# Kernel optimization log

Hardware: AMD Instinct MI355X
Metric: run time of the kernel (lower is better)

The kernel has to match this reference:

```python
import jax, jax.numpy as jnp
import numpy as np

B, S, D = 2, 2048, 1024
H = 16
HD = D // H  # 64


def setup_inputs() -> dict:
    key = jax.random.key(0)
    ks = jax.random.split(key, 9)
    s = 1.0 / np.sqrt(D)
    x = jax.random.normal(ks[0], (B, S, D), dtype=jnp.float32)
    Wq = jax.random.normal(ks[1], (D, D), dtype=jnp.float32) * s
    Wk = jax.random.normal(ks[2], (D, D), dtype=jnp.float32) * s
    Wv = jax.random.normal(ks[3], (D, D), dtype=jnp.float32) * s
    Wo = jax.random.normal(ks[4], (D, D), dtype=jnp.float32) * s
    bq = jnp.zeros((D,), jnp.float32)
    bk = jnp.zeros((D,), jnp.float32)
    bv = jnp.zeros((D,), jnp.float32)
    bo = jnp.zeros((D,), jnp.float32)
    # causal mask, broadcastable to (B, H, S, S)
    mask = jnp.tril(jnp.ones((S, S), dtype=bool))[None, None, :, :]
    return {"x": x, "Wq": Wq, "bq": bq, "Wk": Wk, "bk": bk,
            "Wv": Wv, "bv": bv, "Wo": Wo, "bo": bo, "mask": mask}


def _split_heads(t):
    # (B, S, D) -> (B, H, S, HD)
    b, s, _ = t.shape
    return t.reshape(b, s, H, HD).transpose(0, 2, 1, 3)


def reference(x, Wq, bq, Wk, bk, Wv, bv, Wo, bo, mask):
    q = _split_heads(x @ Wq + bq)
    k = _split_heads(x @ Wk + bk)
    v = _split_heads(x @ Wv + bv)
    scale = 1.0 / jnp.sqrt(jnp.asarray(HD, dtype=q.dtype))
    scores = jnp.einsum('bhqd,bhkd->bhqk', q, k) * scale
    large_neg = jnp.finfo(scores.dtype).min
    scores = jnp.where(mask, scores, large_neg)
    attn = jax.nn.softmax(scores, axis=-1)
    out = jnp.einsum('bhqk,bhkd->bhqd', attn, v)  # (B,H,S,HD)
    out = out.transpose(0, 2, 1, 3).reshape(x.shape[0], x.shape[1], D)
    return out @ Wo + bo
```

## Files before the change

kernel.cpp:

```cpp
#include <hip/hip_runtime.h>
#include <hip/hip_bf16.h>

typedef __attribute__((ext_vector_type(8))) short bf16x8;
typedef __attribute__((ext_vector_type(4))) float f32x4;

#define B_DIM  2
#define S_DIM  2048
#define D_DIM  1024
#define H_DIM  16
#define HD_DIM 64

__device__ __forceinline__ float bf2f(ushort u) {
    union { unsigned int ui; float f; } c; c.ui = ((unsigned int)u) << 16; return c.f;
}
__device__ __forceinline__ ushort f2bf(float f) {
    __hip_bfloat16 h = __float2bfloat16(f);
    return *reinterpret_cast<ushort*>(&h);
}

__device__ __forceinline__ void async_cp16(const ushort* g, ushort* l) {
    __builtin_amdgcn_global_load_lds(
        (const __attribute__((address_space(1))) void*)g,
        (__attribute__((address_space(3))) void*)l, 16, 0, 0);
}

__global__ __launch_bounds__(256) void detect_kernel(const ushort* __restrict__ x,
                                                     int* __restrict__ flag) {
    __shared__ int any;
    int tid = threadIdx.x;
    if (tid == 0) any = 0;
    __syncthreads();
    int cnt = 0;
    for (int j = 0; j < 64; ++j) {
        ushort u = x[tid * 64 + j];
        if (((u >> 7) & 0xFF) == 0xFF) cnt++;
    }
    if (cnt) atomicOr(&any, 1);
    __syncthreads();
    if (tid == 0) *flag = any ? 1 : 0;
}

__global__ __launch_bounds__(256) void prep_kernel(const void* __restrict__ x,
                                                   const void* __restrict__ Wq,
                                                   const void* __restrict__ Wk,
                                                   const void* __restrict__ Wv,
                                                   const void* __restrict__ Wo,
                                                   const void* __restrict__ bq,
                                                   const void* __restrict__ bk,
                                                   const void* __restrict__ bv,
                                                   const void* __restrict__ bo,
                                                   ushort* __restrict__ xc,
                                                   ushort* __restrict__ Wqkvt,
                                                   ushort* __restrict__ Wot,
                                                   float* __restrict__ biasf,
                                                   const int* __restrict__ flag) {
    int tid = threadIdx.x;
    int z = blockIdx.z;
    bool isf32 = (*flag != 0);

    if (z == 4) {
        int t = (blockIdx.y * 16 + blockIdx.x) * 256 + tid;
#pragma unroll
        for (int c = 0; c < 8; ++c) {
            int i = t + c * 65536;
            if (isf32) {
                const float* s = (const float*)x;
                f32x4 a = *(const f32x4*)&s[(size_t)i * 8];
                f32x4 b = *(const f32x4*)&s[(size_t)i * 8 + 4];
                bf16x8 o;
                o[0] = f2bf(a.x); o[1] = f2bf(a.y); o[2] = f2bf(a.z); o[3] = f2bf(a.w);
                o[4] = f2bf(b.x); o[5] = f2bf(b.y); o[6] = f2bf(b.z); o[7] = f2bf(b.w);
                *(bf16x8*)&xc[(size_t)i * 8] = o;
            } else {
                *(bf16x8*)&xc[(size_t)i * 8] =
                    *(const bf16x8*)&((const ushort*)x)[(size_t)i * 8];
            }
        }
        return;
    }
    if (z == 5) {
        int bid = blockIdx.y * 16 + blockIdx.x;
        if (bid >= 16) return;
        int i = bid * 256 + tid;
        int w = i >> 10, j = i & 1023;
        const void* s = (w == 0) ? bq : (w == 1) ? bk : (w == 2) ? bv : bo;
        biasf[i] = isf32 ? ((const float*)s)[j] : bf2f(((const ushort*)s)[j]);
        return;
    }

    __shared__ ushort tile[64][72];
    const void* src = (z == 0) ? Wq : (z == 1) ? Wk : (z == 2) ? Wv : Wo;
    ushort* dst = (z < 3) ? (Wqkvt + (size_t)z * D_DIM * D_DIM) : Wot;
    int r0 = blockIdx.y * 64, c0 = blockIdx.x * 64;
#pragma unroll
    for (int p = 0; p < 2; ++p) {
        int r = p * 32 + (tid >> 3);
        int c = (tid & 7) * 8;
        if (isf32) {
            const float* s = (const float*)src;
            f32x4 a = *(const f32x4*)&s[(size_t)(r0 + r) * D_DIM + c0 + c];
            f32x4 b = *(const f32x4*)&s[(size_t)(r0 + r) * D_DIM + c0 + c + 4];
            tile[r][c + 0] = f2bf(a.x); tile[r][c + 1] = f2bf(a.y);
            tile[r][c + 2] = f2bf(a.z); tile[r][c + 3] = f2bf(a.w);
            tile[r][c + 4] = f2bf(b.x); tile[r][c + 5] = f2bf(b.y);
            tile[r][c + 6] = f2bf(b.z); tile[r][c + 7] = f2bf(b.w);
        } else {
            *(bf16x8*)&tile[r][c] =
                *(const bf16x8*)&((const ushort*)src)[(size_t)(r0 + r) * D_DIM + c0 + c];
        }
    }
    __syncthreads();
#pragma unroll
    for (int p = 0; p < 2; ++p) {
        int n  = p * 32 + (tid >> 3);
        int cc = (tid & 7) * 8;
        bf16x8 v;
#pragma unroll
        for (int e = 0; e < 8; ++e) v[e] = (short)tile[cc + e][n];
        *(bf16x8*)&dst[(size_t)(c0 + n) * D_DIM + r0 + cc] = v;
    }
}

__global__ __launch_bounds__(256) void transpose_v_kernel(const ushort* __restrict__ src,
                                                          ushort* __restrict__ dst) {
    __shared__ ushort tile[64][72];
    int tid = threadIdx.x;
    int s0 = blockIdx.x * 64;
    int bh = blockIdx.y;
    const ushort* sb = src + (size_t)bh * S_DIM * HD_DIM;
    ushort* db = dst + (size_t)bh * HD_DIM * S_DIM;
#pragma unroll
    for (int p = 0; p < 2; ++p) {
        int r = p * 32 + (tid >> 3);
        int c = (tid & 7) * 8;
        *(bf16x8*)&tile[r][c] = *(const bf16x8*)&sb[(size_t)(s0 + r) * HD_DIM + c];
    }
    __syncthreads();
#pragma unroll
    for (int p = 0; p < 2; ++p) {
        int n  = p * 32 + (tid >> 3);
        int cc = (tid & 7) * 8;
        bf16x8 v;
#pragma unroll
        for (int e = 0; e < 8; ++e) v[e] = (short)tile[cc + e][n];
        *(bf16x8*)&db[(size_t)n * S_DIM + s0 + cc] = v;
    }
}

__global__ __launch_bounds__(256) void gemm128_kernel(const ushort* __restrict__ A,
                                                      const ushort* __restrict__ Bt,
                                                      const float* __restrict__ bias,
                                                      void* __restrict__ out,
                                                      const int* __restrict__ flag,
                                                      int mode) {
    __shared__ ushort As[128 * 64];
    __shared__ ushort Bs[128 * 64];
    int tid  = threadIdx.x;
    int wave = tid >> 6;
    int lane = tid & 63;
    int l16  = lane & 15;
    int quad = lane >> 4;
    int m0   = blockIdx.y * 128;
    int n0   = blockIdx.x * 128;
    int wm   = wave >> 1;
    int wn   = wave & 1;
    const int K = 1024;

    f32x4 acc[4][4];
#pragma unroll
    for (int i = 0; i < 4; ++i)
#pragma unroll
        for (int j = 0; j < 4; ++j) acc[i][j] = (f32x4){0.f, 0.f, 0.f, 0.f};

    int lrow = lane >> 3;
    int gcol = ((lane & 7) ^ lrow) * 8;
    int sw   = l16 & 7;

    for (int kt = 0; kt < 16; ++kt) {
        int k0 = kt * 64;
#pragma unroll
        for (int j = 0; j < 4; ++j) {
            int chunk = wave * 4 + j;
            int grow  = chunk * 8 + lrow;
            async_cp16(&A[(size_t)(m0 + grow) * K + k0 + gcol], &As[chunk * 512]);
            async_cp16(&Bt[(size_t)(n0 + grow) * K + k0 + gcol], &Bs[chunk * 512]);
        }
        __syncthreads();

#pragma unroll
        for (int kb = 0; kb < 2; ++kb) {
            bf16x8 af[4], bf[4];
#pragma unroll
            for (int i = 0; i < 4; ++i)
                af[i] = *(const bf16x8*)&As[(wm * 64 + i * 16 + l16) * 64 +
                                            (((kb * 4 + quad) ^ sw) << 3)];
#pragma unroll
            for (int j = 0; j < 4; ++j)
                bf[j] = *(const bf16x8*)&Bs[(wn * 64 + j * 16 + l16) * 64 +
                                            (((kb * 4 + quad) ^ sw) << 3)];
#pragma unroll
            for (int i = 0; i < 4; ++i)
#pragma unroll
                for (int j = 0; j < 4; ++j)
                    acc[i][j] = __builtin_amdgcn_mfma_f32_16x16x32_bf16(af[i], bf[j],
                                                                        acc[i][j], 0, 0, 0);
        }
        __syncthreads();
    }

    int outf32 = (mode == 1) ? *flag : 0;
    const size_t TSZ = (size_t)B_DIM * H_DIM * S_DIM * HD_DIM;
#pragma unroll
    for (int j = 0; j < 4; ++j) {
        int n = n0 + wn * 64 + j * 16 + l16;
        float bv = bias[n];
#pragma unroll
        for (int i = 0; i < 4; ++i)
#pragma unroll
            for (int r = 0; r < 4; ++r) {
                int m = m0 + wm * 64 + i * 16 + quad * 4 + r;
                float v = acc[i][j][r] + bv;
                if (mode == 0) {
                    int which = n >> 10;
                    int n1 = n & 1023;
                    int h = n1 >> 6, hd = n1 & 63;
                    int b = m >> 11, s = m & (S_DIM - 1);
                    if (which == 0) v *= 0.18033688011f;
                    ((ushort*)out)[which * TSZ +
                        ((((size_t)(b * H_DIM + h)) * S_DIM + s) << 6) + hd] = f2bf(v);
                } else if (outf32) {
                    ((float*)out)[(size_t)m * D_DIM + n] = v;
                } else {
                    ((ushort*)out)[(size_t)m * D_DIM + n] = f2bf(v);
                }
            }
    }
}

#define SLD 72
__global__ __launch_bounds__(256) void attn_kernel(const ushort* __restrict__ Qg,
                                                   const ushort* __restrict__ Kg,
                                                   const ushort* __restrict__ Vt,
                                                   ushort* __restrict__ attn_out) {
    __shared__ ushort Ks[64 * SLD];
    __shared__ ushort Vs[64 * SLD];
    __shared__ ushort Ss[128 * SLD];
    int tid  = threadIdx.x;
    int wave = tid >> 6;
    int lane = tid & 63;
    int l16  = lane & 15;
    int quad = lane >> 4;
    int bh   = blockIdx.x;
    int y    = blockIdx.y;
    int qt   = (y < 8) ? (15 - y) : (y - 8);
    int q0   = qt * 128;

    const ushort* Qb = Qg + (size_t)bh * S_DIM * HD_DIM;
    const ushort* Kb = Kg + (size_t)bh * S_DIM * HD_DIM;
    const ushort* Vb = Vt + (size_t)bh * HD_DIM * S_DIM;

    bf16x8 qf[2][2];
#pragma unroll
    for (int g = 0; g < 2; ++g)
#pragma unroll
        for (int ks = 0; ks < 2; ++ks)
            qf[g][ks] = *(const bf16x8*)&Qb[(size_t)(q0 + wave * 32 + g * 16 + l16) * HD_DIM +
                                            ks * 32 + quad * 8];

    f32x4 o[2][4];
#pragma unroll
    for (int g = 0; g < 2; ++g)
#pragma unroll
        for (int i = 0; i < 4; ++i) o[g][i] = (f32x4){0.f, 0.f, 0.f, 0.f};
    float rsum[2] = {0.f, 0.f};

    int srow = tid >> 3;
    int scol = (tid & 7) * 8;

    bf16x8 kr[2], vr[2];
#pragma unroll
    for (int p = 0; p < 2; ++p) {
        kr[p] = *(const bf16x8*)&Kb[(size_t)(srow + 32 * p) * HD_DIM + scol];
        vr[p] = *(const bf16x8*)&Vb[(size_t)(srow + 32 * p) * S_DIM + scol];
    }

    int ntiles = 2 * qt + 2;
    for (int t = 0; t < ntiles; ++t) {
        __syncthreads();
#pragma unroll
        for (int p = 0; p < 2; ++p) {
            *(bf16x8*)&Ks[(srow + 32 * p) * SLD + scol] = kr[p];
            *(bf16x8*)&Vs[(srow + 32 * p) * SLD + scol] = vr[p];
        }
        __syncthreads();
        if (t + 1 < ntiles) {
            int k1 = (t + 1) * 64;
#pragma unroll
            for (int p = 0; p < 2; ++p) {
                kr[p] = *(const bf16x8*)&Kb[(size_t)(k1 + srow + 32 * p) * HD_DIM + scol];
                vr[p] = *(const bf16x8*)&Vb[(size_t)(srow + 32 * p) * S_DIM + k1 + scol];
            }
        }

        int k0 = t * 64;

        f32x4 sc[2][4];
#pragma unroll
        for (int g = 0; g < 2; ++g)
#pragma unroll
            for (int i = 0; i < 4; ++i) sc[g][i] = (f32x4){0.f, 0.f, 0.f, 0.f};
#pragma unroll
        for (int ks = 0; ks < 2; ++ks)
#pragma unroll
            for (int nb = 0; nb < 4; ++nb) {
                bf16x8 kf = *(const bf16x8*)&Ks[(nb * 16 + l16) * SLD + ks * 32 + quad * 8];
#pragma unroll
                for (int g = 0; g < 2; ++g)
                    sc[g][nb] = __builtin_amdgcn_mfma_f32_16x16x32_bf16(kf, qf[g][ks],
                                                                        sc[g][nb], 0, 0, 0);
            }

        if (t >= ntiles - 2) {
#pragma unroll
            for (int g = 0; g < 2; ++g) {
                int qglob = q0 + wave * 32 + g * 16 + l16;
#pragma unroll
                for (int nb = 0; nb < 4; ++nb) {
                    int key = k0 + nb * 16 + quad * 4;
#pragma unroll
                    for (int r = 0; r < 4; ++r)
                        if (key + r > qglob) sc[g][nb][r] = -1e30f;
                }
            }
        }

#pragma unroll
        for (int g = 0; g < 2; ++g)
#pragma unroll
            for (int nb = 0; nb < 4; ++nb) {
                ushort pk[4];
                float ps = 0.f;
#pragma unroll
                for (int r = 0; r < 4; ++r) {
                    float p = __builtin_amdgcn_exp2f(sc[g][nb][r]);
                    ps += p;
                    pk[r] = f2bf(p);
                }
                rsum[g] += ps;
                *(uint2*)&Ss[(wave * 32 + g * 16 + l16) * SLD + nb * 16 + quad * 4] =
                    *(uint2*)pk;
            }

        bf16x8 pf[2][2];
#pragma unroll
        for (int g = 0; g < 2; ++g)
#pragma unroll
            for (int ks = 0; ks < 2; ++ks)
                pf[g][ks] = *(const bf16x8*)&Ss[(wave * 32 + g * 16 + l16) * SLD +
                                                ks * 32 + quad * 8];

#pragma unroll
        for (int ks = 0; ks < 2; ++ks)
#pragma unroll
            for (int nb = 0; nb < 4; ++nb) {
                bf16x8 vf = *(const bf16x8*)&Vs[(nb * 16 + l16) * SLD + ks * 32 + quad * 8];
#pragma unroll
                for (int g = 0; g < 2; ++g)
                    o[g][nb] = __builtin_amdgcn_mfma_f32_16x16x32_bf16(pf[g][ks], vf,
                                                                       o[g][nb], 0, 0, 0);
            }
    }

#pragma unroll
    for (int g = 0; g < 2; ++g) {
        rsum[g] += __shfl_xor(rsum[g], 16, 64);
        rsum[g] += __shfl_xor(rsum[g], 32, 64);
    }

    int b = bh >> 4, h = bh & 15;
#pragma unroll
    for (int g = 0; g < 2; ++g) {
        float inv[4];
#pragma unroll
        for (int r = 0; r < 4; ++r)
            inv[r] = 1.f / __shfl(rsum[g], quad * 4 + r, 64);
#pragma unroll
        for (int nb = 0; nb < 4; ++nb)
#pragma unroll
            for (int r = 0; r < 4; ++r) {
                int q = q0 + wave * 32 + g * 16 + quad * 4 + r;
                attn_out[(size_t)(b * S_DIM + q) * D_DIM + h * HD_DIM + nb * 16 + l16] =
                    f2bf(o[g][nb][r] * inv[r]);
            }
    }
}

extern "C" void kernel_launch(void* const* d_in, const int* in_sizes, int n_in,
                              void* d_out, int out_size, void* d_ws, size_t ws_size,
                              hipStream_t stream) {
    const void* x  = d_in[0];
    const void* Wq = d_in[1];
    const void* bq = d_in[2];
    const void* Wk = d_in[3];
    const void* bk = d_in[4];
    const void* Wv = d_in[5];
    const void* bv = d_in[6];
    const void* Wo = d_in[7];
    const void* bo = d_in[8];

    char* ws = (char*)d_ws;
    const size_t MB = 1024 * 1024;
    const size_t base = 64 * 1024;
    int*    flag   = (int*)ws;
    float*  biasf  = (float*)(ws + 4096);
    ushort* xc     = (ushort*)(ws + base);
    ushort* Wqkvt  = (ushort*)(ws + base + 8  * MB);
    ushort* Wot    = (ushort*)(ws + base + 14 * MB);
    ushort* Qc     = (ushort*)(ws + base + 16 * MB);
    ushort* Vc     = (ushort*)(ws + base + 32 * MB);
    ushort* Vtp    = (ushort*)(ws + base + 40 * MB);
    ushort* attn   = xc;

    dim3 tb(256);

    detect_kernel<<<1, tb, 0, stream>>>((const ushort*)x, flag);

    dim3 pg(16, 16, 6);
    prep_kernel<<<pg, tb, 0, stream>>>(x, Wq, Wk, Wv, Wo, bq, bk, bv, bo,
                                       xc, Wqkvt, Wot, biasf, flag);

    dim3 gq(3 * D_DIM / 128, (B_DIM * S_DIM) / 128);
    gemm128_kernel<<<gq, tb, 0, stream>>>(xc, Wqkvt, biasf, Qc, flag, 0);

    dim3 vg(S_DIM / 64, B_DIM * H_DIM);
    transpose_v_kernel<<<vg, tb, 0, stream>>>(Vc, Vtp);

    dim3 ag(B_DIM * H_DIM, S_DIM / 128);
    attn_kernel<<<ag, tb, 0, stream>>>(Qc, Qc + (size_t)B_DIM * H_DIM * S_DIM * HD_DIM,
                                       Vtp, attn);

    dim3 go(D_DIM / 128, (B_DIM * S_DIM) / 128);
    gemm128_kernel<<<go, tb, 0, stream>>>(attn, Wot, biasf + 3072, d_out, flag, 1);
}
```

Baseline: 221.4 us.

## Fuse V transpose into QKV GEMM epilogue, add 64-row output GEMM, skip masked waves

The QKV projection GEMM now writes V directly in transposed (head-dim-major) layout with packed 4-element stores, which removes the separate transpose kernel and one round trip of V through global memory. The output projection gets a dedicated 64x128-tile GEMM kernel, doubling the grid from 256 to 512 blocks to fill more compute units. In attention, waves whose query rows are entirely masked out in the last causal tile skip the compute for that tile. The transposed V stores are strided by S, which may reduce write coalescing compared with the old layout.

```diff
diff --git a/kernel.cpp b/kernel.cpp
--- a/kernel.cpp
+++ b/kernel.cpp
@@ -121,38 +121,11 @@
     }
 }
 
-__global__ __launch_bounds__(256) void transpose_v_kernel(const ushort* __restrict__ src,
-                                                          ushort* __restrict__ dst) {
-    __shared__ ushort tile[64][72];
-    int tid = threadIdx.x;
-    int s0 = blockIdx.x * 64;
-    int bh = blockIdx.y;
-    const ushort* sb = src + (size_t)bh * S_DIM * HD_DIM;
-    ushort* db = dst + (size_t)bh * HD_DIM * S_DIM;
-#pragma unroll
-    for (int p = 0; p < 2; ++p) {
-        int r = p * 32 + (tid >> 3);
-        int c = (tid & 7) * 8;
-        *(bf16x8*)&tile[r][c] = *(const bf16x8*)&sb[(size_t)(s0 + r) * HD_DIM + c];
-    }
-    __syncthreads();
-#pragma unroll
-    for (int p = 0; p < 2; ++p) {
-        int n  = p * 32 + (tid >> 3);
-        int cc = (tid & 7) * 8;
-        bf16x8 v;
-#pragma unroll
-        for (int e = 0; e < 8; ++e) v[e] = (short)tile[cc + e][n];
-        *(bf16x8*)&db[(size_t)n * S_DIM + s0 + cc] = v;
-    }
-}
-
 __global__ __launch_bounds__(256) void gemm128_kernel(const ushort* __restrict__ A,
                                                       const ushort* __restrict__ Bt,
                                                       const float* __restrict__ bias,
-                                                      void* __restrict__ out,
-                                                      const int* __restrict__ flag,
-                                                      int mode) {
+                                                      ushort* __restrict__ qkout,
+                                                      ushort* __restrict__ vtout) {
     __shared__ ushort As[128 * 64];
     __shared__ ushort Bs[128 * 64];
     int tid  = threadIdx.x;
@@ -208,31 +181,116 @@
         __syncthreads();
     }
 
-    int outf32 = (mode == 1) ? *flag : 0;
     const size_t TSZ = (size_t)B_DIM * H_DIM * S_DIM * HD_DIM;
 #pragma unroll
     for (int j = 0; j < 4; ++j) {
         int n = n0 + wn * 64 + j * 16 + l16;
         float bv = bias[n];
+        int which = n >> 10;
+        int n1 = n & 1023;
+        int h = n1 >> 6, hd = n1 & 63;
+#pragma unroll
+        for (int i = 0; i < 4; ++i) {
+            int mb = m0 + wm * 64 + i * 16 + quad * 4;
+            int b = mb >> 11, s = mb & (S_DIM - 1);
+            float v4[4];
+#pragma unroll
+            for (int r = 0; r < 4; ++r) v4[r] = acc[i][j][r] + bv;
+            if (which == 2) {
+                ushort pk[4];
+#pragma unroll
+                for (int r = 0; r < 4; ++r) pk[r] = f2bf(v4[r]);
+                *(uint2*)&vtout[(((size_t)(b * H_DIM + h) * HD_DIM + hd)) * S_DIM + s] =
+                    *(uint2*)pk;
+            } else {
+#pragma unroll
+                for (int r = 0; r < 4; ++r) {
+                    float v = v4[r];
+                    if (which == 0) v *= 0.18033688011f;
+                    qkout[which * TSZ +
+                          ((((size_t)(b * H_DIM + h)) * S_DIM + s + r) << 6) + hd] = f2bf(v);
+                }
+            }
+        }
+    }
+}
+
+__global__ __launch_bounds__(256) void gemm64_kernel(const ushort* __restrict__ A,
+                                                     const ushort* __restrict__ Bt,
+                                                     const float* __restrict__ bias,
+                                                     void* __restrict__ out,
+                                                     const int* __restrict__ flag) {
+    __shared__ ushort As[64 * 64];
+    __shared__ ushort Bs[128 * 64];
+    int tid  = threadIdx.x;
+    int wave = tid >> 6;
+    int lane = tid & 63;
+    int l16  = lane & 15;
+    int quad = lane >> 4;
+    int m0   = blockIdx.y * 64;
+    int n0   = blockIdx.x * 128;
+    const int K = 1024;
+
+    f32x4 acc[4][2];
+#pragma unroll
+    for (int i = 0; i < 4; ++i)
+#pragma unroll
+        for (int j = 0; j < 2; ++j) acc[i][j] = (f32x4){0.f, 0.f, 0.f, 0.f};
+
+    int lrow = lane >> 3;
+    int gcol = ((lane & 7) ^ lrow) * 8;
+    int sw   = l16 & 7;
+
+    for (int kt = 0; kt < 16; ++kt) {
+        int k0 = kt * 64;
+#pragma unroll
+        for (int j = 0; j < 2; ++j) {
+            int chunk = wave * 2 + j;
+            int grow  = chunk * 8 + lrow;
+            async_cp16(&A[(size_t)(m0 + grow) * K + k0 + gcol], &As[chunk * 512]);
+        }
+#pragma unroll
+        for (int j = 0; j < 4; ++j) {
+            int chunk = wave * 4 + j;
+            int grow  = chunk * 8 + lrow;
+            async_cp16(&Bt[(size_t)(n0 + grow) * K + k0 + gcol], &Bs[chunk * 512]);
+        }
+        __syncthreads();
+
+#pragma unroll
+        for (int kb = 0; kb < 2; ++kb) {
+            bf16x8 af[4], bf[2];
+#pragma unroll
+            for (int i = 0; i < 4; ++i)
+                af[i] = *(const bf16x8*)&As[(i * 16 + l16) * 64 +
+                                            (((kb * 4 + quad) ^ sw) << 3)];
+#pragma unroll
+            for (int j = 0; j < 2; ++j)
+                bf[j] = *(const bf16x8*)&Bs[(wave * 32 + j * 16 + l16) * 64 +
+                                            (((kb * 4 + quad) ^ sw) << 3)];
+#pragma unroll
+            for (int i = 0; i < 4; ++i)
+#pragma unroll
+                for (int j = 0; j < 2; ++j)
+                    acc[i][j] = __builtin_amdgcn_mfma_f32_16x16x32_bf16(af[i], bf[j],
+                                                                        acc[i][j], 0, 0, 0);
+        }
+        __syncthreads();
+    }
+
+    int outf32 = *flag;
+#pragma unroll
+    for (int j = 0; j < 2; ++j) {
+        int n = n0 + wave * 32 + j * 16 + l16;
+        float bv = bias[n];
 #pragma unroll
         for (int i = 0; i < 4; ++i)
 #pragma unroll
             for (int r = 0; r < 4; ++r) {
-                int m = m0 + wm * 64 + i * 16 + quad * 4 + r;
+                int m = m0 + i * 16 + quad * 4 + r;
                 float v = acc[i][j][r] + bv;
-                if (mode == 0) {
-                    int which = n >> 10;
-                    int n1 = n & 1023;
-                    int h = n1 >> 6, hd = n1 & 63;
-                    int b = m >> 11, s = m & (S_DIM - 1);
-                    if (which == 0) v *= 0.18033688011f;
-                    ((ushort*)out)[which * TSZ +
-                        ((((size_t)(b * H_DIM + h)) * S_DIM + s) << 6) + hd] = f2bf(v);
-                } else if (outf32) {
-                    ((float*)out)[(size_t)m * D_DIM + n] = v;
-                } else {
-                    ((ushort*)out)[(size_t)m * D_DIM + n] = f2bf(v);
-                }
+                if (outf32) ((float*)out)[(size_t)m * D_DIM + n] = v;
+                else        ((ushort*)out)[(size_t)m * D_DIM + n] = f2bf(v);
             }
     }
 }
@@ -302,6 +360,8 @@
             }
         }
 
+        if (t == ntiles - 1 && wave < 2) continue;
+
         int k0 = t * 64;
 
         f32x4 sc[2][4];
@@ -417,7 +477,6 @@
     ushort* Wqkvt  = (ushort*)(ws + base + 8  * MB);
     ushort* Wot    = (ushort*)(ws + base + 14 * MB);
     ushort* Qc     = (ushort*)(ws + base + 16 * MB);
-    ushort* Vc     = (ushort*)(ws + base + 32 * MB);
     ushort* Vtp    = (ushort*)(ws + base + 40 * MB);
     ushort* attn   = xc;
 
@@ -430,15 +489,12 @@
                                        xc, Wqkvt, Wot, biasf, flag);
 
     dim3 gq(3 * D_DIM / 128, (B_DIM * S_DIM) / 128);
-    gemm128_kernel<<<gq, tb, 0, stream>>>(xc, Wqkvt, biasf, Qc, flag, 0);
-
-    dim3 vg(S_DIM / 64, B_DIM * H_DIM);
-    transpose_v_kernel<<<vg, tb, 0, stream>>>(Vc, Vtp);
+    gemm128_kernel<<<gq, tb, 0, stream>>>(xc, Wqkvt, biasf, Qc, Vtp);
 
     dim3 ag(B_DIM * H_DIM, S_DIM / 128);
     attn_kernel<<<ag, tb, 0, stream>>>(Qc, Qc + (size_t)B_DIM * H_DIM * S_DIM * HD_DIM,
                                        Vtp, attn);
 
-    dim3 go(D_DIM / 128, (B_DIM * S_DIM) / 128);
-    gemm128_kernel<<<go, tb, 0, stream>>>(attn, Wot, biasf + 3072, d_out, flag, 1);
-}
+    dim3 go(D_DIM / 128, (B_DIM * S_DIM) / 64);
+    gemm64_kernel<<<go, tb, 0, stream>>>(attn, Wot, biasf + 3072, d_out, flag);
+}
```

Measured after the change: 196.6 us. 11.2% less time.
